# Performance work log

Measured on AMD Instinct MI355X. Metric: run time of the kernel, lower is better.

The kernel has to match this reference:

```python
import jax, jax.numpy as jnp
import numpy as np

N_HEAD, N, F_IN, F_OUT = 8, 4096, 128, 128


def setup_inputs() -> dict:
    key = jax.random.key(0)
    k1, k2, k3, k4 = jax.random.split(key, 4)
    return {
        "h": jax.random.normal(k1, (N, F_IN), dtype=jnp.float32),
        "w": jax.random.normal(k2, (N_HEAD, F_IN, F_OUT), dtype=jnp.float32) * 0.1,
        "a_src": jax.random.normal(k3, (N_HEAD, F_OUT, 1), dtype=jnp.float32) * 0.1,
        "a_dst": jax.random.normal(k4, (N_HEAD, F_OUT, 1), dtype=jnp.float32) * 0.1,
        "bias": jnp.zeros((F_OUT,), dtype=jnp.float32),
        "idx": 0,
    }


def reference(h, w, a_src, a_dst, bias, idx):
    # h: [n, f_in], w: [H, f_in, f_out] -> h_prime: [H, n, f_out]
    h_prime = jnp.einsum("ni,hio->hno", h, w)
    # per-node scalar scores per head: [H, n]
    attn_src = jnp.einsum("hno,ho->hn", h_prime, a_src[..., 0])
    attn_dst = jnp.einsum("hno,ho->hn", h_prime, a_dst[..., 0])
    # dense additive attention: [H, n, n] (src broadcast over cols + dst over rows)
    attn = attn_src[:, :, None] + attn_dst[:, None, :]
    attn = jax.nn.leaky_relu(attn, negative_slope=0.2)
    attn = jax.nn.softmax(attn, axis=-1)
    # dropout is identity in eval mode
    out = jnp.einsum("hnm,hmo->hno", attn, h_prime)  # [H, n, f_out]
    return out.mean(axis=0) + bias  # [n, f_out]
```

## Files before the change

kernel.cpp:

```cpp
#include <hip/hip_runtime.h>
#include <math.h>

#define NH 8
#define NN 4096
#define FF 128
#define SEG 64
#define NSEG (NN / SEG)

typedef unsigned long long u64;

__global__ __launch_bounds__(256) void k1_gemm(
    const float* __restrict__ h, const float* __restrict__ w,
    const float* __restrict__ a_src, const float* __restrict__ a_dst,
    float* __restrict__ hp, float* __restrict__ attn_src,
    float* __restrict__ attn_dst) {
  __shared__ float sw[32 * 128];
  __shared__ float shT[32 * 32];
  const int head = blockIdx.y;
  const int r0 = blockIdx.x * 32;
  const int tid = threadIdx.x;
  const int ty = tid >> 5;
  const int tx = tid & 31;

  float acc[4][4];
  #pragma unroll
  for (int i = 0; i < 4; ++i)
    #pragma unroll
    for (int j = 0; j < 4; ++j) acc[i][j] = 0.f;

  const float4* wg = reinterpret_cast<const float4*>(w + (size_t)head * 128 * 128);
  const float4* hg = reinterpret_cast<const float4*>(h);

  for (int kc = 0; kc < 4; ++kc) {
    const int k0 = kc * 32;
    __syncthreads();
    #pragma unroll
    for (int it = 0; it < 4; ++it) {
      int q = tid + it * 256;
      int krow = q >> 5, c4 = q & 31;
      float4 v = wg[(size_t)(k0 + krow) * 32 + c4];
      float* dst = &sw[krow * 128 + c4 * 4];
      dst[0] = v.x; dst[1] = v.y; dst[2] = v.z; dst[3] = v.w;
    }
    {
      int row = tid >> 3, k4 = tid & 7;
      float4 v = hg[(size_t)(r0 + row) * 32 + (k0 >> 2) + k4];
      #pragma unroll
      for (int j = 0; j < 4; ++j) {
        int kl = k4 * 4 + j;
        int rsw = row ^ (((kl >> 2) & 7) << 2);
        shT[kl * 32 + rsw] = (&v.x)[j];
      }
    }
    __syncthreads();
    #pragma unroll 8
    for (int kk = 0; kk < 32; ++kk) {
      float4 a4 = *reinterpret_cast<const float4*>(
          &shT[kk * 32 + ((ty ^ ((kk >> 2) & 7)) << 2)]);
      float4 b4 = *reinterpret_cast<const float4*>(&sw[kk * 128 + tx * 4]);
      #pragma unroll
      for (int ri = 0; ri < 4; ++ri) {
        float av = (&a4.x)[ri];
        acc[ri][0] += av * b4.x;
        acc[ri][1] += av * b4.y;
        acc[ri][2] += av * b4.z;
        acc[ri][3] += av * b4.w;
      }
    }
  }

  const int rbase = r0 + ty * 4;
  float4* hp4 = reinterpret_cast<float4*>(hp);
  #pragma unroll
  for (int ri = 0; ri < 4; ++ri) {
    hp4[((size_t)(head * NN + rbase + ri)) * 32 + tx] =
        make_float4(acc[ri][0], acc[ri][1], acc[ri][2], acc[ri][3]);
  }
  float4 As = reinterpret_cast<const float4*>(a_src + head * FF)[tx];
  float4 Ad = reinterpret_cast<const float4*>(a_dst + head * FF)[tx];
  #pragma unroll
  for (int ri = 0; ri < 4; ++ri) {
    float sA = acc[ri][0] * As.x + acc[ri][1] * As.y + acc[ri][2] * As.z +
               acc[ri][3] * As.w;
    float sD = acc[ri][0] * Ad.x + acc[ri][1] * Ad.y + acc[ri][2] * Ad.z +
               acc[ri][3] * Ad.w;
    #pragma unroll
    for (int m = 1; m < 32; m <<= 1) {
      sA += __shfl_xor(sA, m);
      sD += __shfl_xor(sD, m);
    }
    if (tx == 0) {
      attn_src[head * NN + rbase + ri] = sA;
      attn_dst[head * NN + rbase + ri] = sD;
    }
  }
}

__global__ __launch_bounds__(256) void k2a_localsort(
    const float* __restrict__ adst, u64* __restrict__ runs) {
  __shared__ u64 sk[512];
  const int head = blockIdx.y, chunk = blockIdx.x, tid = threadIdx.x;
  const int base = head * NN + chunk * 512;
  for (int i = tid; i < 512; i += 256) {
    unsigned ub = __float_as_uint(adst[base + i]);
    unsigned u = (ub & 0x80000000u) ? ~ub : (ub | 0x80000000u);
    sk[i] = ((u64)u << 32) | (unsigned)(chunk * 512 + i);
  }
  __syncthreads();
  for (int k = 2; k <= 512; k <<= 1) {
    for (int j = k >> 1; j > 0; j >>= 1) {
      for (int t = tid; t < 512; t += 256) {
        int ixj = t ^ j;
        if (ixj > t) {
          u64 a = sk[t], b = sk[ixj];
          bool up = ((t & k) == 0);
          if (up ? (a > b) : (a < b)) { sk[t] = b; sk[ixj] = a; }
        }
      }
      __syncthreads();
    }
  }
  for (int i = tid; i < 512; i += 256) runs[base + i] = sk[i];
}

template <int L, bool FINAL>
__global__ __launch_bounds__(256) void k2m(
    const u64* __restrict__ src, u64* __restrict__ dst,
    float* __restrict__ dsort, int* __restrict__ permd) {
  const int head = blockIdx.y;
  const int i = (blockIdx.x * 256 + threadIdx.x) * 4;
  const u64* S = src + head * NN;
  const int region = i / (2 * L), q0 = i % (2 * L);
  const u64* A = S + region * 2 * L;
  const u64* B = A + L;
  int lo = q0 > L ? q0 - L : 0, hi = q0 < L ? q0 : L;
  while (lo < hi) {
    int mid = (lo + hi) >> 1;
    if (A[mid] < B[q0 - 1 - mid]) lo = mid + 1; else hi = mid;
  }
  int a = lo, b = q0 - lo;
  #pragma unroll
  for (int t = 0; t < 4; ++t) {
    u64 va = a < L ? A[a] : ~0ULL;
    u64 vb = b < L ? B[b] : ~0ULL;
    u64 v;
    if (va < vb) { v = va; ++a; } else { v = vb; ++b; }
    const int q = region * 2 * L + q0 + t;
    if (FINAL) {
      unsigned u = (unsigned)(v >> 32);
      unsigned ub = (u & 0x80000000u) ? (u ^ 0x80000000u) : ~u;
      dsort[head * NN + q] = __uint_as_float(ub);
      permd[head * NN + q] = (int)(v & 0xffffffffu);
    } else {
      dst[head * NN + q] = v;
    }
  }
}

__global__ __launch_bounds__(256) void k3_segsum(
    const float* __restrict__ hp, const float* __restrict__ dsort,
    const int* __restrict__ permd, float* __restrict__ segs,
    float* __restrict__ segz) {
  __shared__ float se0[SEG], se1[SEG];
  __shared__ int sp[SEG];
  __shared__ float comb[2 * FF];
  const int head = blockIdx.y, seg = blockIdx.x;
  const int tid = threadIdx.x;
  const int o = tid & 127, jh = tid >> 7;
  {
    int t = tid & 63;
    float dv = dsort[head * NN + seg * SEG + t];
    if (tid < 64) {
      se0[t] = expf(0.2f * dv);
      sp[t] = permd[head * NN + seg * SEG + t];
    } else if (tid < 128) {
      se1[t] = expf(dv);
    }
  }
  __syncthreads();
  const float* hph = hp + (size_t)head * NN * FF;
  float a0 = 0.f, a1 = 0.f;
  #pragma unroll 8
  for (int u = 0; u < 32; ++u) {
    int jj = u * 2 + jh;
    float hv = hph[(size_t)sp[jj] * FF + o];
    a0 += se0[jj] * hv;
    a1 += se1[jj] * hv;
  }
  if (jh == 1) {
    comb[o] = a0;
    comb[FF + o] = a1;
  }
  __syncthreads();
  if (jh == 0) {
    a0 += comb[o];
    a1 += comb[FF + o];
    size_t base = ((size_t)(head * NSEG + seg)) * 2 * FF;
    segs[base + o] = a0;
    segs[base + FF + o] = a1;
    if (o == 0) {
      float zz0 = 0.f, zz1 = 0.f;
      #pragma unroll
      for (int j = 0; j < SEG; ++j) { zz0 += se0[j]; zz1 += se1[j]; }
      segz[(head * NSEG + seg) * 2 + 0] = zz0;
      segz[(head * NSEG + seg) * 2 + 1] = zz1;
    }
  }
}

__global__ __launch_bounds__(128) void k5_prefix(
    const float* __restrict__ hp, const float* __restrict__ dsort,
    const int* __restrict__ permd, const float* __restrict__ segs,
    const float* __restrict__ segz, float* __restrict__ PF,
    float* __restrict__ PFz) {
  __shared__ float se0[SEG], se1[SEG];
  __shared__ int sp[SEG];
  const int head = blockIdx.y, seg = blockIdx.x;
  const int o = threadIdx.x;
  {
    int t = o & 63;
    float dv = dsort[head * NN + seg * SEG + t];
    if (o < 64) {
      se0[t] = expf(0.2f * dv);
      sp[t] = permd[head * NN + seg * SEG + t];
    } else {
      se1[t] = expf(dv);
    }
  }
  __syncthreads();
  float r0 = 0.f, r1 = 0.f, z0 = 0.f, z1 = 0.f;
  const float* sbase = segs + ((size_t)head * NSEG) * 2 * FF;
  #pragma unroll 4
  for (int k = 0; k < seg; ++k) {
    r0 += sbase[(size_t)k * 2 * FF + o];
    r1 += sbase[(size_t)k * 2 * FF + FF + o];
  }
  #pragma unroll 4
  for (int k = 0; k < seg; ++k) {
    z0 += segz[(head * NSEG + k) * 2 + 0];
    z1 += segz[(head * NSEG + k) * 2 + 1];
  }
  const float* hph = hp + (size_t)head * NN * FF;
  #pragma unroll 4
  for (int jj = 0; jj < SEG; ++jj) {
    int j = seg * SEG + jj;
    float hv = hph[(size_t)sp[jj] * FF + o];
    float e0 = se0[jj], e1 = se1[jj];
    r0 += e0 * hv;
    r1 += e1 * hv;
    z0 += e0;
    z1 += e1;
    size_t pb = ((size_t)(head * NN + j)) * 2 * FF;
    PF[pb + o] = r0;
    PF[pb + FF + o] = r1;
    if (o == 0) {
      PFz[(head * NN + j) * 2 + 0] = z0;
      PFz[(head * NN + j) * 2 + 1] = z1;
    }
  }
}

__global__ __launch_bounds__(128) void k6_out(
    const float* __restrict__ attn_src, const float* __restrict__ dsort,
    const float* __restrict__ PF, const float* __restrict__ PFz,
    const float* __restrict__ bias, float* __restrict__ out) {
  __shared__ int st[NH];
  __shared__ float ss[NH];
  const int n = blockIdx.x, o = threadIdx.x;
  if (o < NH) {
    float s = attn_src[o * NN + n];
    ss[o] = s;
    const float* dp = dsort + o * NN;
    float thr = -s;
    int lo = 0, hi = NN;
    while (lo < hi) {
      int mid = (lo + hi) >> 1;
      if (dp[mid] <= thr) lo = mid + 1; else hi = mid;
    }
    st[o] = lo;
  }
  __syncthreads();
  float acc = 0.f;
  #pragma unroll
  for (int head = 0; head < NH; ++head) {
    float s = ss[head];
    int t = st[head];
    size_t tb = ((size_t)(head * NN + NN - 1)) * 2 * FF;
    float TotA = PF[tb + FF + o];
    float z1tot = PFz[(head * NN + NN - 1) * 2 + 1];
    float B = 0.f, P1 = 0.f, z0p = 0.f, z1p = 0.f;
    if (t > 0) {
      size_t pb = ((size_t)(head * NN + t - 1)) * 2 * FF;
      B = PF[pb + o];
      P1 = PF[pb + FF + o];
      z0p = PFz[(head * NN + t - 1) * 2 + 0];
      z1p = PFz[(head * NN + t - 1) * 2 + 1];
    }
    float e02s = expf(0.2f * s), es = expf(s);
    float den = e02s * z0p + es * (z1tot - z1p);
    acc += (e02s * B + es * (TotA - P1)) / den;
  }
  out[(size_t)n * FF + o] = 0.125f * acc + bias[o];
}

extern "C" void kernel_launch(void* const* d_in, const int* in_sizes, int n_in,
                              void* d_out, int out_size, void* d_ws,
                              size_t ws_size, hipStream_t stream) {
  const float* h = (const float*)d_in[0];
  const float* w = (const float*)d_in[1];
  const float* a_src = (const float*)d_in[2];
  const float* a_dst = (const float*)d_in[3];
  const float* bias = (const float*)d_in[4];
  float* out = (float*)d_out;

  char* ws = (char*)d_ws;
  size_t off = 0;
  auto alloc = [&](size_t bytes) -> void* {
    void* p = ws + off;
    off += (bytes + 255) & ~(size_t)255;
    return p;
  };
  float* hp = (float*)alloc((size_t)NH * NN * FF * 4);
  float* asrc = (float*)alloc((size_t)NH * NN * 4);
  float* adst = (float*)alloc((size_t)NH * NN * 4);
  float* dsort = (float*)alloc((size_t)NH * NN * 4);
  int* permd = (int*)alloc((size_t)NH * NN * 4);
  float* segs = (float*)alloc((size_t)NH * NSEG * 2 * FF * 4);
  float* segz = (float*)alloc((size_t)NH * NSEG * 2 * 4);
  float* PF = (float*)alloc((size_t)NH * NN * 2 * FF * 4);
  float* PFz = (float*)alloc((size_t)NH * NN * 2 * 4);
  u64* sbuf0 = (u64*)alloc((size_t)NH * NN * 8);
  u64* sbuf1 = (u64*)alloc((size_t)NH * NN * 8);
  (void)ws_size;

  k1_gemm<<<dim3(NN / 32, NH), 256, 0, stream>>>(h, w, a_src, a_dst, hp, asrc,
                                                 adst);
  k2a_localsort<<<dim3(8, NH), 256, 0, stream>>>(adst, sbuf0);
  k2m<512, false><<<dim3(4, NH), 256, 0, stream>>>(sbuf0, sbuf1, nullptr,
                                                   nullptr);
  k2m<1024, false><<<dim3(4, NH), 256, 0, stream>>>(sbuf1, sbuf0, nullptr,
                                                    nullptr);
  k2m<2048, true><<<dim3(4, NH), 256, 0, stream>>>(sbuf0, nullptr, dsort,
                                                   permd);
  k3_segsum<<<dim3(NSEG, NH), 256, 0, stream>>>(hp, dsort, permd, segs, segz);
  k5_prefix<<<dim3(NSEG, NH), 128, 0, stream>>>(hp, dsort, permd, segs, segz,
                                                PF, PFz);
  k6_out<<<NN, 128, 0, stream>>>(asrc, dsort, PF, PFz, bias, out);
}
```

Baseline: 161.6 us.

## Halve prefix segment size and hoist binary-search thresholds into separate kernel

The segment size drops from 64 to 32, which doubles the number of blocks in the segment-sum and prefix kernels and halves each block's serial scan length. The per-node binary search over sorted dst scores moves out of the output kernel into a new fully parallel kernel that writes positions to a workspace buffer. The output kernel then no longer runs a serial search on only 8 threads followed by a block barrier. In exchange there is one extra launch and a longer serial loop over preceding segment sums in the prefix kernel.

```diff
diff --git a/kernel.cpp b/kernel.cpp
--- a/kernel.cpp
+++ b/kernel.cpp
@@ -4,7 +4,7 @@
 #define NH 8
 #define NN 4096
 #define FF 128
-#define SEG 64
+#define SEG 32
 #define NSEG (NN / SEG)
 
 typedef unsigned long long u64;
@@ -167,21 +167,20 @@
   const int head = blockIdx.y, seg = blockIdx.x;
   const int tid = threadIdx.x;
   const int o = tid & 127, jh = tid >> 7;
-  {
-    int t = tid & 63;
-    float dv = dsort[head * NN + seg * SEG + t];
-    if (tid < 64) {
-      se0[t] = expf(0.2f * dv);
-      sp[t] = permd[head * NN + seg * SEG + t];
-    } else if (tid < 128) {
-      se1[t] = expf(dv);
-    }
+  const int sbse = head * NN + seg * SEG;
+  if (tid < SEG) {
+    float dv = dsort[sbse + tid];
+    se0[tid] = expf(0.2f * dv);
+    sp[tid] = permd[sbse + tid];
+  } else if (tid < 2 * SEG) {
+    int t = tid - SEG;
+    se1[t] = expf(dsort[sbse + t]);
   }
   __syncthreads();
   const float* hph = hp + (size_t)head * NN * FF;
   float a0 = 0.f, a1 = 0.f;
-  #pragma unroll 8
-  for (int u = 0; u < 32; ++u) {
+  #pragma unroll
+  for (int u = 0; u < SEG / 2; ++u) {
     int jj = u * 2 + jh;
     float hv = hph[(size_t)sp[jj] * FF + o];
     a0 += se0[jj] * hv;
@@ -208,6 +207,21 @@
   }
 }
 
+__global__ __launch_bounds__(256) void k4_thresh(
+    const float* __restrict__ attn_src, const float* __restrict__ dsort,
+    int* __restrict__ tpos) {
+  const int i = blockIdx.x * 256 + threadIdx.x;
+  const int head = i >> 12, n = i & (NN - 1);
+  const float thr = -attn_src[head * NN + n];
+  const float* dp = dsort + head * NN;
+  int lo = 0, hi = NN;
+  while (lo < hi) {
+    int mid = (lo + hi) >> 1;
+    if (dp[mid] <= thr) lo = mid + 1; else hi = mid;
+  }
+  tpos[i] = lo;
+}
+
 __global__ __launch_bounds__(128) void k5_prefix(
     const float* __restrict__ hp, const float* __restrict__ dsort,
     const int* __restrict__ permd, const float* __restrict__ segs,
@@ -217,31 +231,30 @@
   __shared__ int sp[SEG];
   const int head = blockIdx.y, seg = blockIdx.x;
   const int o = threadIdx.x;
-  {
-    int t = o & 63;
-    float dv = dsort[head * NN + seg * SEG + t];
-    if (o < 64) {
-      se0[t] = expf(0.2f * dv);
-      sp[t] = permd[head * NN + seg * SEG + t];
-    } else {
-      se1[t] = expf(dv);
-    }
+  const int sbse = head * NN + seg * SEG;
+  if (o < SEG) {
+    float dv = dsort[sbse + o];
+    se0[o] = expf(0.2f * dv);
+    sp[o] = permd[sbse + o];
+  } else if (o < 2 * SEG) {
+    int t = o - SEG;
+    se1[t] = expf(dsort[sbse + t]);
   }
   __syncthreads();
   float r0 = 0.f, r1 = 0.f, z0 = 0.f, z1 = 0.f;
   const float* sbase = segs + ((size_t)head * NSEG) * 2 * FF;
-  #pragma unroll 4
+  #pragma unroll 8
   for (int k = 0; k < seg; ++k) {
     r0 += sbase[(size_t)k * 2 * FF + o];
     r1 += sbase[(size_t)k * 2 * FF + FF + o];
   }
-  #pragma unroll 4
+  #pragma unroll 8
   for (int k = 0; k < seg; ++k) {
     z0 += segz[(head * NSEG + k) * 2 + 0];
     z1 += segz[(head * NSEG + k) * 2 + 1];
   }
   const float* hph = hp + (size_t)head * NN * FF;
-  #pragma unroll 4
+  #pragma unroll 8
   for (int jj = 0; jj < SEG; ++jj) {
     int j = seg * SEG + jj;
     float hv = hph[(size_t)sp[jj] * FF + o];
@@ -261,30 +274,15 @@
 }
 
 __global__ __launch_bounds__(128) void k6_out(
-    const float* __restrict__ attn_src, const float* __restrict__ dsort,
+    const float* __restrict__ attn_src, const int* __restrict__ tpos,
     const float* __restrict__ PF, const float* __restrict__ PFz,
     const float* __restrict__ bias, float* __restrict__ out) {
-  __shared__ int st[NH];
-  __shared__ float ss[NH];
   const int n = blockIdx.x, o = threadIdx.x;
-  if (o < NH) {
-    float s = attn_src[o * NN + n];
-    ss[o] = s;
-    const float* dp = dsort + o * NN;
-    float thr = -s;
-    int lo = 0, hi = NN;
-    while (lo < hi) {
-      int mid = (lo + hi) >> 1;
-      if (dp[mid] <= thr) lo = mid + 1; else hi = mid;
-    }
-    st[o] = lo;
-  }
-  __syncthreads();
   float acc = 0.f;
   #pragma unroll
   for (int head = 0; head < NH; ++head) {
-    float s = ss[head];
-    int t = st[head];
+    float s = attn_src[head * NN + n];
+    int t = tpos[head * NN + n];
     size_t tb = ((size_t)(head * NN + NN - 1)) * 2 * FF;
     float TotA = PF[tb + FF + o];
     float z1tot = PFz[(head * NN + NN - 1) * 2 + 1];
@@ -325,6 +323,7 @@
   float* adst = (float*)alloc((size_t)NH * NN * 4);
   float* dsort = (float*)alloc((size_t)NH * NN * 4);
   int* permd = (int*)alloc((size_t)NH * NN * 4);
+  int* tpos = (int*)alloc((size_t)NH * NN * 4);
   float* segs = (float*)alloc((size_t)NH * NSEG * 2 * FF * 4);
   float* segz = (float*)alloc((size_t)NH * NSEG * 2 * 4);
   float* PF = (float*)alloc((size_t)NH * NN * 2 * FF * 4);
@@ -343,7 +342,8 @@
   k2m<2048, true><<<dim3(4, NH), 256, 0, stream>>>(sbuf0, nullptr, dsort,
                                                    permd);
   k3_segsum<<<dim3(NSEG, NH), 256, 0, stream>>>(hp, dsort, permd, segs, segz);
+  k4_thresh<<<NH * NN / 256, 256, 0, stream>>>(asrc, dsort, tpos);
   k5_prefix<<<dim3(NSEG, NH), 128, 0, stream>>>(hp, dsort, permd, segs, segz,
                                                 PF, PFz);
-  k6_out<<<NN, 128, 0, stream>>>(asrc, dsort, PF, PFz, bias, out);
-}
+  k6_out<<<NN, 128, 0, stream>>>(asrc, tpos, PF, PFz, bias, out);
+}
```

Result: no change. 162.2 us (+0.3%).
